# Kernel optimization log

Hardware: AMD Instinct MI355X
Metric: run time of the kernel (lower is better)

## Reference

```python
import jax, jax.numpy as jnp
import numpy as np

B, C, H, W = 256, 3, 224, 224
NP, PS = 14, 16          # patches per row, patch size
D, NH, NB = 192, 4, 3    # hidden_d, num_heads (Block default), n_blocks
OUT = 1000
T = NP * NP + 1          # tokens incl. class token


def _lin(x, w, b):
    # torch nn.Linear: y = x @ W^T + b, W is [out, in]
    return x @ w.T + b


def setup_inputs() -> dict:
    key = jax.random.key(0)
    ks = jax.random.split(key, 22)
    n = lambda k, shp: jax.random.normal(k, shp, dtype=jnp.float32) * 0.02
    return {
        "x": jax.random.normal(ks[0], (B, C, H, W), dtype=jnp.float32),
        "lm_w": n(ks[1], (D, C * PS * PS)), "lm_b": n(ks[2], (D,)),
        "cls_tok": jax.random.uniform(ks[3], (1, D), dtype=jnp.float32),  # torch.rand
        "pos_emb": n(ks[4], (T, D)),
        # per-block params stacked on leading dim NB
        "q_w": n(ks[5], (NB, D, D)), "q_b": n(ks[6], (NB, D)),
        "k_w": n(ks[7], (NB, D, D)), "k_b": n(ks[8], (NB, D)),
        "v_w": n(ks[9], (NB, D, D)), "v_b": n(ks[10], (NB, D)),
        "in_w": n(ks[11], (NB, 3 * D, D)), "in_b": n(ks[12], (NB, 3 * D)),
        "out_w": n(ks[13], (NB, D, D)), "out_b": n(ks[14], (NB, D)),
        "up_w": n(ks[15], (NB, 4 * D, D)), "up_b": n(ks[16], (NB, 4 * D)),
        "down_w": n(ks[17], (NB, D, 4 * D)), "down_b": n(ks[18], (NB, D)),
        "head_w": n(ks[19], (OUT, D)), "head_b": n(ks[20], (OUT,)),
    }


def reference(x, lm_w, lm_b, cls_tok, pos_emb, q_w, q_b, k_w, k_b, v_w, v_b,
              in_w, in_b, out_w, out_b, up_w, up_b, down_w, down_b, head_w, head_b):
    N = x.shape[0]
    # vectorized patchify: [N,C,H,W] -> [N, NP*NP, C*PS*PS] (flatten order C,ps,ps matches torch)
    patches = x.reshape(N, C, NP, PS, NP, PS).transpose(0, 2, 4, 1, 3, 5).reshape(N, NP * NP, C * PS * PS)
    tok = _lin(patches, lm_w, lm_b)
    tok = jnp.concatenate([jnp.broadcast_to(cls_tok[None], (N, 1, D)), tok], axis=1) + pos_emb[None]
    dh = D // NH
    scale = 1.0 / np.sqrt(dh).astype(np.float32)
    for i in range(NB):
        # Block's own q/k/v projections
        q = _lin(tok, q_w[i], q_b[i])
        k = _lin(tok, k_w[i], k_b[i])
        v = _lin(tok, v_w[i], v_b[i])
        # nn.MultiheadAttention internal in_proj (applied on top of q/k/v)
        wq, wk, wv = jnp.split(in_w[i], 3, axis=0)
        bq, bk, bv = jnp.split(in_b[i], 3, axis=0)
        qh = _lin(q, wq, bq).reshape(N, T, NH, dh).transpose(0, 2, 1, 3)
        kh = _lin(k, wk, bk).reshape(N, T, NH, dh).transpose(0, 2, 1, 3)
        vh = _lin(v, wv, bv).reshape(N, T, NH, dh).transpose(0, 2, 1, 3)
        scores = jnp.einsum('bhqd,bhkd->bhqk', qh, kh) * scale
        attn = jax.nn.softmax(scores, axis=-1)
        o = jnp.einsum('bhqk,bhkd->bhqd', attn, vh).transpose(0, 2, 1, 3).reshape(N, T, D)
        o = _lin(o, out_w[i], out_b[i])  # MHA out_proj
        tok = tok + o                     # residual around attention only
        tok = _lin(jax.nn.relu(_lin(tok, up_w[i], up_b[i])), down_w[i], down_b[i])  # MLP, no residual
    cls = tok[:, 0, :]
    return _lin(cls, head_w, head_b)
```

## Files before the change

### kernel.cpp

```cpp
#include <hip/hip_runtime.h>

typedef unsigned short u16;
typedef __bf16 bf16x8 __attribute__((ext_vector_type(8)));
typedef float  f32x4  __attribute__((ext_vector_type(4)));
typedef u16    u16x8  __attribute__((ext_vector_type(8)));

#define BATCH 256
#define TT    197
#define TP    256
#define DD    192
#define DHP   64
#define MTOK  (BATCH*TT)
#define MPAT  (BATCH*196)

constexpr size_t BIG_E  = 1024ull*256*256;
constexpr size_t TOK_E  = (size_t)MTOK*DD;
constexpr size_t QKV_E  = 1024ull*TP*DHP;

__device__ __forceinline__ float b2f(u16 h){ union{unsigned u; float f;} x; x.u=(unsigned)h<<16; return x.f; }
__device__ __forceinline__ u16 f2b(float f){ union{float f; unsigned u;} x{f}; unsigned r = x.u + 0x7fffu + ((x.u>>16)&1u); return (u16)(r>>16); }
__device__ __forceinline__ bf16x8 as_bf(u16x8 v){ return __builtin_bit_cast(bf16x8, v); }

__device__ __forceinline__ void gload_lds16(const void* g, void* l) {
  __builtin_amdgcn_global_load_lds((__attribute__((address_space(1))) void*)(size_t)g,
                                   (__attribute__((address_space(3))) void*)l, 16, 0, 0);
}

enum { M_F32=0, M_BF16=1, M_QKV=2, M_PATCH=4 };

template<int MODE, bool RELU, bool RES, bool BIAS>
__global__ __launch_bounds__(256)
void gemm4w(const u16* __restrict__ A, const u16* __restrict__ W,
            const float* __restrict__ bias, const u16* __restrict__ res,
            void* __restrict__ Cout, const float* __restrict__ aux,
            int K, int lda, int ldc, int Nreal,
            long bA, long bW, long bC)
{
  __shared__ __align__(16) u16 As[3][128*32];
  __shared__ __align__(16) u16 Ws[3][64*32];
  const int tid  = threadIdx.x;
  const int wv   = tid >> 6;
  const int lane = tid & 63;

  const int nN  = gridDim.x, nM = gridDim.y;
  const int nwg = nN * nM;
  const int fid = blockIdx.x + nN * blockIdx.y;
  const int xcd = fid & 7, loc = fid >> 3;
  const int q8  = nwg >> 3, r8 = nwg & 7;
  const int tile = (xcd < r8 ? xcd * (q8 + 1) : r8 * (q8 + 1) + (xcd - r8) * q8) + loc;
  const int m0 = (tile / nN) * 128;
  const int n0 = (tile % nN) * 64;

  const int bz = blockIdx.z;
  const u16* Ab = A + (size_t)bz * (size_t)bA;
  const u16* Wb = W + (size_t)bz * (size_t)bW;

  const int lrow = lane & 15, quad = lane >> 4;
  const int srow = lane >> 2, sseg = lane & 3;
  const int wsw  = (srow >> 1) & 3;
  const int rsw  = (lrow >> 1) & 3;

  f32x4 acc[2][4];
  #pragma unroll
  for (int i=0;i<2;i++)
    #pragma unroll
    for (int j=0;j<4;j++) { f32x4 z = {0.f,0.f,0.f,0.f}; acc[i][j] = z; }

  auto stage = [&](int bufi, int k0) {
    #pragma unroll
    for (int i=0;i<2;i++) {
      const u16* ga = Ab + (size_t)(m0 + i*64 + wv*16 + srow)*lda + (k0 + (sseg^wsw)*8);
      gload_lds16(ga, &As[bufi][(i*64 + wv*16)*32]);
    }
    const u16* gw = Wb + (size_t)(n0 + wv*16 + srow)*K + (k0 + (sseg^wsw)*8);
    gload_lds16(gw, &Ws[bufi][(wv*16)*32]);
  };

  const int nt = K >> 5;
  stage(0, 0);
  stage(1, 32);
  for (int t = 0; t < nt; ++t) {
    if (t + 1 < nt) {
      asm volatile("s_waitcnt vmcnt(3)" ::: "memory");
    } else {
      asm volatile("s_waitcnt vmcnt(0)" ::: "memory");
    }
    asm volatile("s_barrier" ::: "memory");
    if (t + 2 < nt) stage((t + 2) % 3, (t + 2) << 5);

    const int cur = t % 3;
    bf16x8 af[2], wf[4];
    #pragma unroll
    for (int i=0;i<2;i++)
      af[i] = *(const bf16x8*)&As[cur][(wv*32 + i*16 + lrow)*32 + (quad^rsw)*8];
    #pragma unroll
    for (int i=0;i<4;i++)
      wf[i] = *(const bf16x8*)&Ws[cur][(i*16 + lrow)*32 + (quad^rsw)*8];
    #pragma unroll
    for (int mi=0;mi<2;mi++)
      #pragma unroll
      for (int ni=0;ni<4;ni++)
        acc[mi][ni] = __builtin_amdgcn_mfma_f32_16x16x32_bf16(af[mi], wf[ni], acc[mi][ni], 0,0,0);
  }

  #pragma unroll
  for (int mi=0;mi<2;mi++) {
    #pragma unroll
    for (int ni=0;ni<4;ni++) {
      #pragma unroll
      for (int r=0;r<4;r++) {
        int row = m0 + wv*32 + mi*16 + quad*4 + r;
        int col = n0 + ni*16 + lrow;
        float v = acc[mi][ni][r];
        if constexpr (MODE == M_F32) {
          if (col < Nreal) {
            if constexpr (BIAS) v += bias[col];
            ((float*)Cout)[(size_t)row*ldc + col] = v;
          }
        } else if constexpr (MODE == M_BF16) {
          if constexpr (BIAS) v += bias[col];
          if constexpr (RES)  v += b2f(res[(size_t)row*ldc + col]);
          if constexpr (RELU) v = v > 0.f ? v : 0.f;
          ((u16*)Cout)[(size_t)bz*(size_t)bC + (size_t)row*ldc + col] = f2b(v);
        } else if constexpr (MODE == M_QKV) {
          v += bias[col];
          int sel = col / 192, rem = col % 192;
          int h = rem / 48, d = rem % 48;
          int b = row / 197, t = row % 197;
          ((u16*)Cout)[(size_t)sel*QKV_E + ((size_t)(b*4 + h)*TP + t)*DHP + d] = f2b(v);
        } else if constexpr (MODE == M_PATCH) {
          int b = row / 196, p = row % 196;
          v += bias[col] + aux[(size_t)(1 + p)*DD + col];
          ((u16*)Cout)[((size_t)(b*197) + 1 + p)*DD + col] = f2b(v);
        }
      }
    }
  }
}

#define KSTR 72
#define VSTR 216
#define PSTR 72
#define TKR  208

__global__ __launch_bounds__(256,1)
void flash_k(const u16* __restrict__ Qg, const u16* __restrict__ Kg,
             const u16* __restrict__ Vg, u16* __restrict__ Og)
{
  __shared__ __align__(16) u16 Ks[TKR*KSTR];
  __shared__ __align__(16) u16 Vs[49*VSTR];
  __shared__ __align__(16) u16 Ps[8*16*PSTR];
  const int bh = blockIdx.x;
  const int b = bh >> 2, h = bh & 3;
  const int tid = threadIdx.x, wv = tid >> 6, lane = tid & 63;
  const int lrow = lane & 15, quad = lane >> 4;
  const size_t base = (size_t)bh * TP * DHP;
  const float scale = 0.14433756729740643f;

  bf16x8 qf[4][2];
  #pragma unroll
  for (int rg=0; rg<4; rg++)
    #pragma unroll
    for (int ka=0; ka<2; ka++)
      qf[rg][ka] = as_bf(*(const u16x8*)(Qg + base + (size_t)(wv*64+rg*16+lrow)*DHP + ka*32 + quad*8));

  for (int it=0; it<5; it++) {
    int slot = it*256 + tid;
    if (slot < 1248) {
      int t = slot/6, sg = slot - t*6;
      u16x8 v = *(const u16x8*)(Kg + base + (size_t)t*DHP + sg*8);
      *(u16x8*)&Ks[t*KSTR + sg*8] = v;
    }
  }
  {
    u16x8 z = {0,0,0,0,0,0,0,0};
    for (int it=0; it<2; it++) {
      int slot = it*256 + tid;
      if (slot < 416) { int t = slot>>1, sg = 6 + (slot&1);
        *(u16x8*)&Ks[t*KSTR + sg*8] = z; }
    }
  }
  for (int it=0; it<5; it++) {
    int slot = it*256 + tid;
    if (slot < 1248) {
      int sg = slot/208, t = slot - sg*208;
      u16x8 v = *(const u16x8*)(Vg + base + (size_t)t*DHP + sg*8);
      #pragma unroll
      for (int j=0;j<8;j++) Vs[(sg*8+j)*VSTR + t] = v[j];
    }
  }
  __syncthreads();

  f32x4 o[4][3];
  float m_i[4][4], l_i[4][4];
  #pragma unroll
  for (int rg=0;rg<4;rg++) {
    #pragma unroll
    for (int dg=0;dg<3;dg++) { f32x4 z = {0.f,0.f,0.f,0.f}; o[rg][dg] = z; }
    #pragma unroll
    for (int r=0;r<4;r++) { m_i[rg][r] = -1e30f; l_i[rg][r] = 0.f; }
  }
  u16* PwA = &Ps[(wv*2 + 0)*16*PSTR];
  u16* PwB = &Ps[(wv*2 + 1)*16*PSTR];

  #pragma unroll
  for (int c=0; c<4; c++) {
    const int NC = (c<3) ? 4 : 1;
    f32x4 s[4][4];
    #pragma unroll
    for (int rg=0;rg<4;rg++)
      #pragma unroll
      for (int cg=0;cg<4;cg++) if (cg < NC) { f32x4 z = {0.f,0.f,0.f,0.f}; s[rg][cg] = z; }

    #pragma unroll
    for (int cg=0;cg<4;cg++) if (cg < NC) {
      #pragma unroll
      for (int ka=0; ka<2; ka++) {
        bf16x8 kf = as_bf(*(const u16x8*)&Ks[(c*64+cg*16+lrow)*KSTR + ka*32 + quad*8]);
        #pragma unroll
        for (int rg=0;rg<4;rg++)
          s[rg][cg] = __builtin_amdgcn_mfma_f32_16x16x32_bf16(qf[rg][ka], kf, s[rg][cg], 0,0,0);
      }
    }

    #pragma unroll
    for (int rg=0;rg<4;rg++) {
      const int it  = c*4 + rg;
      if (c == 3) {
        #pragma unroll
        for (int r=0;r<4;r++) s[rg][0][r] = (lrow >= 5) ? -1e30f : s[rg][0][r];
      }
      float mnew[4], al[4];
      #pragma unroll
      for (int r=0;r<4;r++) {
        float mc = s[rg][0][r];
        #pragma unroll
        for (int cg=1;cg<4;cg++) if (cg < NC) mc = fmaxf(mc, s[rg][cg][r]);
        #pragma unroll
        for (int sh=1; sh<16; sh<<=1) mc = fmaxf(mc, __shfl_xor(mc, sh, 64));
        float mo = m_i[rg][r];
        float mn = fmaxf(mo, mc);
        mnew[r] = mn;
        al[r] = __expf((mo - mn)*scale);
      }
      #pragma unroll
      for (int r=0;r<4;r++) {
        float acc = 0.f;
        #pragma unroll
        for (int cg=0;cg<4;cg++) if (cg < NC) {
          float p = __expf((s[rg][cg][r] - mnew[r])*scale);
          s[rg][cg][r] = p;
          acc += p;
        }
        #pragma unroll
        for (int sh=1; sh<16; sh<<=1) acc += __shfl_xor(acc, sh, 64);
        l_i[rg][r] = l_i[rg][r]*al[r] + acc;
        m_i[rg][r] = mnew[r];
      }

      if (it > 0) {
        const int pit = it - 1, ppc = pit >> 2, pprg = pit & 3;
        const int NKp = (ppc < 3) ? 2 : 1;
        const u16* Pr = (pit & 1) ? PwB : PwA;
        __builtin_amdgcn_s_waitcnt(0xC07F);
        #pragma unroll
        for (int ka=0; ka<2; ka++) if (ka < NKp) {
          bf16x8 pf = as_bf(*(const u16x8*)&Pr[lrow*PSTR + ka*32 + quad*8]);
          #pragma unroll
          for (int dg=0;dg<3;dg++) {
            bf16x8 vf = as_bf(*(const u16x8*)&Vs[(dg*16+lrow)*VSTR + ppc*64 + ka*32 + quad*8]);
            o[pprg][dg] = __builtin_amdgcn_mfma_f32_16x16x32_bf16(pf, vf, o[pprg][dg], 0,0,0);
          }
        }
      }

      #pragma unroll
      for (int dg=0;dg<3;dg++)
        #pragma unroll
        for (int r=0;r<4;r++) o[rg][dg][r] *= al[r];

      u16* Pd = (it & 1) ? PwB : PwA;
      #pragma unroll
      for (int cg=0;cg<4;cg++) if (cg < NC) {
        #pragma unroll
        for (int r=0;r<4;r++)
          Pd[(quad*4+r)*PSTR + cg*16 + lrow] = f2b(s[rg][cg][r]);
      }
      if (c == 3) {
        #pragma unroll
        for (int r=0;r<4;r++) Pd[(quad*4+r)*PSTR + 16 + lrow] = 0;
      }
    }
  }
  {
    __builtin_amdgcn_s_waitcnt(0xC07F);
    bf16x8 pf = as_bf(*(const u16x8*)&PwB[lrow*PSTR + quad*8]);
    #pragma unroll
    for (int dg=0;dg<3;dg++) {
      bf16x8 vf = as_bf(*(const u16x8*)&Vs[(dg*16+lrow)*VSTR + 3*64 + quad*8]);
      o[3][dg] = __builtin_amdgcn_mfma_f32_16x16x32_bf16(pf, vf, o[3][dg], 0,0,0);
    }
  }

  #pragma unroll
  for (int rg=0;rg<4;rg++) {
    #pragma unroll
    for (int r=0;r<4;r++) {
      int t = wv*64 + rg*16 + quad*4 + r;
      if (t < 197) {
        float inv = 1.0f / l_i[rg][r];
        u16* dst = Og + ((size_t)(b*197) + t)*DD + h*48;
        #pragma unroll
        for (int dg=0;dg<3;dg++) dst[dg*16 + lrow] = f2b(o[rg][dg][r]*inv);
      }
    }
  }
}

__global__ void cvt5_k(const float* __restrict__ a, const float* __restrict__ b,
                       const float* __restrict__ c, const float* __restrict__ d,
                       const float* __restrict__ e,
                       u16* __restrict__ oa, u16* __restrict__ ob, u16* __restrict__ oc,
                       u16* __restrict__ od, u16* __restrict__ oe) {
  int i = blockIdx.x*256 + threadIdx.x;
  if (i < 147456) { oa[i] = f2b(a[i]); return; } i -= 147456;
  if (i < 110592) { ob[i] = f2b(b[i]); return; } i -= 110592;
  if (i < 442368) { oc[i] = f2b(c[i]); return; } i -= 442368;
  if (i < 442368) { od[i] = f2b(d[i]); return; } i -= 442368;
  if (i < 196608) { oe[i] = (i < 192000) ? f2b(e[i]) : (u16)0; }
}

__global__ void im2col_k(const float* __restrict__ x, u16* __restrict__ P) {
  int id = blockIdx.x*256 + threadIdx.x;
  int w8 = id % 28; int r = id / 28;
  int h  = r % 224; r /= 224;
  int c  = r % 3;   int b = r / 3;
  const float* src = x + (((size_t)(b*3 + c)*224 + h)*224 + w8*8);
  float4 a  = *(const float4*)src;
  float4 bb = *(const float4*)(src + 4);
  int pr = h >> 4, i = h & 15, pc = (w8*8) >> 4, j0 = (w8*8) & 15;
  u16* dst = P + ((size_t)(b*196) + pr*14 + pc)*768 + (c*256 + i*16 + j0);
  u16x8 o;
  o[0]=f2b(a.x); o[1]=f2b(a.y); o[2]=f2b(a.z); o[3]=f2b(a.w);
  o[4]=f2b(bb.x); o[5]=f2b(bb.y); o[6]=f2b(bb.z); o[7]=f2b(bb.w);
  *(u16x8*)dst = o;
}

__global__ void cls_k(const float* __restrict__ cls_tok, const float* __restrict__ pos, u16* __restrict__ tok) {
  int b = blockIdx.x, d = threadIdx.x;
  tok[((size_t)b*197)*DD + d] = f2b(cls_tok[d] + pos[d]);
}

__global__ void fusew_k(const float* __restrict__ in_w, const float* __restrict__ q_w,
                        const float* __restrict__ k_w, const float* __restrict__ v_w,
                        u16* __restrict__ weff) {
  int i = blockIdx.x, p = blockIdx.y, n = blockIdx.z;
  int k = threadIdx.x;
  const float* wrow = in_w + ((size_t)i*576 + p*192 + n)*192;
  const float* Bm = (p==0 ? q_w : (p==1 ? k_w : v_w)) + (size_t)i*192*192;
  float acc = 0.f;
  for (int m=0;m<192;m++) acc += wrow[m] * Bm[m*192 + k];
  weff[((size_t)i*576 + p*192 + n)*192 + k] = f2b(acc);
}

__global__ void fuseb_k(const float* __restrict__ in_w, const float* __restrict__ q_b,
                        const float* __restrict__ k_b, const float* __restrict__ v_b,
                        const float* __restrict__ in_b, float* __restrict__ effb) {
  int i = blockIdx.x, n = threadIdx.x;
  int p = n / 192;
  const float* bb = (p==0 ? q_b : (p==1 ? k_b : v_b)) + i*192;
  const float* wrow = in_w + ((size_t)i*576 + n)*192;
  float acc = in_b[i*576 + n];
  for (int m=0;m<192;m++) acc += wrow[m]*bb[m];
  effb[i*576 + n] = acc;
}

extern "C" void kernel_launch(void* const* d_in, const int* in_sizes, int n_in,
                              void* d_out, int out_size, void* d_ws, size_t ws_size,
                              hipStream_t stream) {
  const float* x      = (const float*)d_in[0];
  const float* lm_w   = (const float*)d_in[1];
  const float* lm_b   = (const float*)d_in[2];
  const float* cls_t  = (const float*)d_in[3];
  const float* pos    = (const float*)d_in[4];
  const float* q_w    = (const float*)d_in[5];
  const float* q_b    = (const float*)d_in[6];
  const float* k_w    = (const float*)d_in[7];
  const float* k_b    = (const float*)d_in[8];
  const float* v_w    = (const float*)d_in[9];
  const float* v_b    = (const float*)d_in[10];
  const float* in_w   = (const float*)d_in[11];
  const float* in_b   = (const float*)d_in[12];
  const float* out_w  = (const float*)d_in[13];
  const float* out_b  = (const float*)d_in[14];
  const float* up_w   = (const float*)d_in[15];
  const float* up_b   = (const float*)d_in[16];
  const float* dn_w   = (const float*)d_in[17];
  const float* dn_b   = (const float*)d_in[18];
  const float* head_w = (const float*)d_in[19];
  const float* head_b = (const float*)d_in[20];

  char* ws = (char*)d_ws;
  size_t off = 0;
  auto alloc = [&](size_t elems, size_t esz) {
    void* p = ws + off; off += ((elems*esz + 255)/256)*256; return p;
  };
  u16*  big  = (u16*)alloc(BIG_E, 2);
  u16*  tok  = (u16*)alloc(TOK_E, 2);
  u16*  qq   = (u16*)alloc(QKV_E*3, 2);
  u16*  obuf = (u16*)alloc(TOK_E, 2);
  u16*  lmw  = (u16*)alloc(147456, 2);
  u16*  outw = (u16*)alloc(110592, 2);
  u16*  upw  = (u16*)alloc(442368, 2);
  u16*  dnw  = (u16*)alloc(442368, 2);
  u16*  hdw  = (u16*)alloc(196608, 2);
  u16*  weff = (u16*)alloc(331776, 2);
  float* effb = (float*)alloc(1728, 4);
  (void)ws_size; (void)in_sizes; (void)n_in; (void)out_size;

  u16* kbuf = qq + QKV_E;
  u16* vbuf = qq + 2*QKV_E;

  cvt5_k<<<(1339392+255)/256,256,0,stream>>>(lm_w, out_w, up_w, dn_w, head_w,
                                             lmw, outw, upw, dnw, hdw);
  fusew_k<<<dim3(3,3,192),192,0,stream>>>(in_w, q_w, k_w, v_w, weff);
  fuseb_k<<<3,576,0,stream>>>(in_w, q_b, k_b, v_b, in_b, effb);

  im2col_k<<<18816,256,0,stream>>>(x, big);
  gemm4w<M_PATCH,false,false,true><<<dim3(3,MPAT/128,1),256,0,stream>>>(
      big, lmw, lm_b, nullptr, tok, pos, 768, 768, DD, DD, 0,0,0);
  cls_k<<<BATCH,DD,0,stream>>>(cls_t, pos, tok);

  for (int i=0;i<3;i++) {
    gemm4w<M_QKV,false,false,true><<<dim3(9,MTOK/128,1),256,0,stream>>>(
        tok, weff + (size_t)i*576*192, effb + i*576, nullptr, qq, nullptr,
        192, 192, 0, 576, 0,0,0);
    flash_k<<<1024,256,0,stream>>>(qq, kbuf, vbuf, obuf);
    gemm4w<M_BF16,false,true,true><<<dim3(3,MTOK/128,1),256,0,stream>>>(
        obuf, outw + (size_t)i*36864, out_b + i*192, tok, tok, nullptr,
        192, 192, DD, DD, 0,0,0);
    gemm4w<M_BF16,true,false,true><<<dim3(12,MTOK/128,1),256,0,stream>>>(
        tok, upw + (size_t)i*147456, up_b + i*768, nullptr, big, nullptr,
        192, 192, 768, 768, 0,0,0);
    gemm4w<M_BF16,false,false,true><<<dim3(3,MTOK/128,1),256,0,stream>>>(
        big, dnw + (size_t)i*147456, dn_b + i*192, nullptr, tok, nullptr,
        768, 768, DD, DD, 0,0,0);
  }
  gemm4w<M_F32,false,false,true><<<dim3(16,2,1),256,0,stream>>>(
      tok, hdw, head_b, nullptr, d_out, nullptr,
      192, 197*192, 1000, 1000, 0,0,0);
}
```

Baseline: 973.8 us.

## Split flash attention rows across eight waves and drop PV software pipelining

The attention kernel now launches 512 threads per block. Each wave owns 32 query rows instead of 64, and the wave whose rows all fall past the 197 valid tokens exits after the shared K/V load. The P·V product now runs right after each P tile is written, using one P buffer per wave instead of the double-buffered one-step-delayed pipeline. This is meant to raise wave-level parallelism, cut per-wave register pressure and reduce wasted padded rows. In exchange it loses the overlap between softmax and the previous tile's P·V MFMAs.

```diff
diff --git a/kernel.cpp b/kernel.cpp
--- a/kernel.cpp
+++ b/kernel.cpp
@@ -143,7 +143,7 @@
 #define PSTR 72
 #define TKR  208
 
-__global__ __launch_bounds__(256,1)
+__global__ __launch_bounds__(512)
 void flash_k(const u16* __restrict__ Qg, const u16* __restrict__ Kg,
              const u16* __restrict__ Vg, u16* __restrict__ Og)
 {
@@ -157,15 +157,16 @@
   const size_t base = (size_t)bh * TP * DHP;
   const float scale = 0.14433756729740643f;
 
-  bf16x8 qf[4][2];
-  #pragma unroll
-  for (int rg=0; rg<4; rg++)
+  bf16x8 qf[2][2];
+  #pragma unroll
+  for (int rg=0; rg<2; rg++)
     #pragma unroll
     for (int ka=0; ka<2; ka++)
-      qf[rg][ka] = as_bf(*(const u16x8*)(Qg + base + (size_t)(wv*64+rg*16+lrow)*DHP + ka*32 + quad*8));
-
-  for (int it=0; it<5; it++) {
-    int slot = it*256 + tid;
+      qf[rg][ka] = as_bf(*(const u16x8*)(Qg + base + (size_t)(wv*32+rg*16+lrow)*DHP + ka*32 + quad*8));
+
+  #pragma unroll
+  for (int it=0; it<3; it++) {
+    int slot = it*512 + tid;
     if (slot < 1248) {
       int t = slot/6, sg = slot - t*6;
       u16x8 v = *(const u16x8*)(Kg + base + (size_t)t*DHP + sg*8);
@@ -174,14 +175,12 @@
   }
   {
     u16x8 z = {0,0,0,0,0,0,0,0};
-    for (int it=0; it<2; it++) {
-      int slot = it*256 + tid;
-      if (slot < 416) { int t = slot>>1, sg = 6 + (slot&1);
-        *(u16x8*)&Ks[t*KSTR + sg*8] = z; }
-    }
-  }
-  for (int it=0; it<5; it++) {
-    int slot = it*256 + tid;
+    if (tid < 416) { int t = tid>>1, sg = 6 + (tid&1);
+      *(u16x8*)&Ks[t*KSTR + sg*8] = z; }
+  }
+  #pragma unroll
+  for (int it=0; it<3; it++) {
+    int slot = it*512 + tid;
     if (slot < 1248) {
       int sg = slot/208, t = slot - sg*208;
       u16x8 v = *(const u16x8*)(Vg + base + (size_t)t*DHP + sg*8);
@@ -190,25 +189,25 @@
     }
   }
   __syncthreads();
-
-  f32x4 o[4][3];
-  float m_i[4][4], l_i[4][4];
-  #pragma unroll
-  for (int rg=0;rg<4;rg++) {
+  if (wv == 7) return;
+
+  f32x4 o[2][3];
+  float m_i[2][4], l_i[2][4];
+  #pragma unroll
+  for (int rg=0;rg<2;rg++) {
     #pragma unroll
     for (int dg=0;dg<3;dg++) { f32x4 z = {0.f,0.f,0.f,0.f}; o[rg][dg] = z; }
     #pragma unroll
     for (int r=0;r<4;r++) { m_i[rg][r] = -1e30f; l_i[rg][r] = 0.f; }
   }
-  u16* PwA = &Ps[(wv*2 + 0)*16*PSTR];
-  u16* PwB = &Ps[(wv*2 + 1)*16*PSTR];
+  u16* Pw = &Ps[wv*16*PSTR];
 
   #pragma unroll
   for (int c=0; c<4; c++) {
     const int NC = (c<3) ? 4 : 1;
-    f32x4 s[4][4];
-    #pragma unroll
-    for (int rg=0;rg<4;rg++)
+    f32x4 s[2][4];
+    #pragma unroll
+    for (int rg=0;rg<2;rg++)
       #pragma unroll
       for (int cg=0;cg<4;cg++) if (cg < NC) { f32x4 z = {0.f,0.f,0.f,0.f}; s[rg][cg] = z; }
 
@@ -218,14 +217,13 @@
       for (int ka=0; ka<2; ka++) {
         bf16x8 kf = as_bf(*(const u16x8*)&Ks[(c*64+cg*16+lrow)*KSTR + ka*32 + quad*8]);
         #pragma unroll
-        for (int rg=0;rg<4;rg++)
+        for (int rg=0;rg<2;rg++)
           s[rg][cg] = __builtin_amdgcn_mfma_f32_16x16x32_bf16(qf[rg][ka], kf, s[rg][cg], 0,0,0);
       }
     }
 
     #pragma unroll
-    for (int rg=0;rg<4;rg++) {
-      const int it  = c*4 + rg;
+    for (int rg=0;rg<2;rg++) {
       if (c == 3) {
         #pragma unroll
         for (int r=0;r<4;r++) s[rg][0][r] = (lrow >= 5) ? -1e30f : s[rg][0][r];
@@ -257,56 +255,42 @@
         l_i[rg][r] = l_i[rg][r]*al[r] + acc;
         m_i[rg][r] = mnew[r];
       }
-
-      if (it > 0) {
-        const int pit = it - 1, ppc = pit >> 2, pprg = pit & 3;
-        const int NKp = (ppc < 3) ? 2 : 1;
-        const u16* Pr = (pit & 1) ? PwB : PwA;
-        __builtin_amdgcn_s_waitcnt(0xC07F);
-        #pragma unroll
-        for (int ka=0; ka<2; ka++) if (ka < NKp) {
-          bf16x8 pf = as_bf(*(const u16x8*)&Pr[lrow*PSTR + ka*32 + quad*8]);
-          #pragma unroll
-          for (int dg=0;dg<3;dg++) {
-            bf16x8 vf = as_bf(*(const u16x8*)&Vs[(dg*16+lrow)*VSTR + ppc*64 + ka*32 + quad*8]);
-            o[pprg][dg] = __builtin_amdgcn_mfma_f32_16x16x32_bf16(pf, vf, o[pprg][dg], 0,0,0);
-          }
+      #pragma unroll
+      for (int dg=0;dg<3;dg++)
+        #pragma unroll
+        for (int r=0;r<4;r++) o[rg][dg][r] *= al[r];
+
+      #pragma unroll
+      for (int cg=0;cg<4;cg++) if (cg < NC) {
+        #pragma unroll
+        for (int r=0;r<4;r++)
+          Pw[(quad*4+r)*PSTR + cg*16 + lrow] = f2b(s[rg][cg][r]);
+      }
+      if (c == 3) {
+        #pragma unroll
+        for (int r=0;r<4;r++) Pw[(quad*4+r)*PSTR + 16 + lrow] = 0;
+      }
+      __builtin_amdgcn_s_waitcnt(0xC07F);
+
+      const int NK = (c<3) ? 2 : 1;
+      #pragma unroll
+      for (int ka=0; ka<2; ka++) if (ka < NK) {
+        bf16x8 pf = as_bf(*(const u16x8*)&Pw[lrow*PSTR + ka*32 + quad*8]);
+        #pragma unroll
+        for (int dg=0;dg<3;dg++) {
+          bf16x8 vf = as_bf(*(const u16x8*)&Vs[(dg*16+lrow)*VSTR + c*64 + ka*32 + quad*8]);
+          o[rg][dg] = __builtin_amdgcn_mfma_f32_16x16x32_bf16(pf, vf, o[rg][dg], 0,0,0);
         }
       }
-
-      #pragma unroll
-      for (int dg=0;dg<3;dg++)
-        #pragma unroll
-        for (int r=0;r<4;r++) o[rg][dg][r] *= al[r];
-
-      u16* Pd = (it & 1) ? PwB : PwA;
-      #pragma unroll
-      for (int cg=0;cg<4;cg++) if (cg < NC) {
-        #pragma unroll
-        for (int r=0;r<4;r++)
-          Pd[(quad*4+r)*PSTR + cg*16 + lrow] = f2b(s[rg][cg][r]);
-      }
-      if (c == 3) {
-        #pragma unroll
-        for (int r=0;r<4;r++) Pd[(quad*4+r)*PSTR + 16 + lrow] = 0;
-      }
-    }
-  }
-  {
-    __builtin_amdgcn_s_waitcnt(0xC07F);
-    bf16x8 pf = as_bf(*(const u16x8*)&PwB[lrow*PSTR + quad*8]);
-    #pragma unroll
-    for (int dg=0;dg<3;dg++) {
-      bf16x8 vf = as_bf(*(const u16x8*)&Vs[(dg*16+lrow)*VSTR + 3*64 + quad*8]);
-      o[3][dg] = __builtin_amdgcn_mfma_f32_16x16x32_bf16(pf, vf, o[3][dg], 0,0,0);
-    }
-  }
-
-  #pragma unroll
-  for (int rg=0;rg<4;rg++) {
+      __builtin_amdgcn_s_waitcnt(0xC07F);
+    }
+  }
+
+  #pragma unroll
+  for (int rg=0;rg<2;rg++) {
     #pragma unroll
     for (int r=0;r<4;r++) {
-      int t = wv*64 + rg*16 + quad*4 + r;
+      int t = wv*32 + rg*16 + quad*4 + r;
       if (t < 197) {
         float inv = 1.0f / l_i[rg][r];
         u16* dst = Og + ((size_t)(b*197) + t)*DD + h*48;
@@ -435,7 +419,7 @@
     gemm4w<M_QKV,false,false,true><<<dim3(9,MTOK/128,1),256,0,stream>>>(
         tok, weff + (size_t)i*576*192, effb + i*576, nullptr, qq, nullptr,
         192, 192, 0, 576, 0,0,0);
-    flash_k<<<1024,256,0,stream>>>(qq, kbuf, vbuf, obuf);
+    flash_k<<<1024,512,0,stream>>>(qq, kbuf, vbuf, obuf);
     gemm4w<M_BF16,false,true,true><<<dim3(3,MTOK/128,1),256,0,stream>>>(
         obuf, outw + (size_t)i*36864, out_b + i*192, tok, tok, nullptr,
         192, 192, DD, DD, 0,0,0);
```

Measured after the change: 881.4 us. 9.5% less time.
